# Kernel optimization log

Measured on AMD Instinct MI355X. Metric: run time of the kernel, lower is better.

The kernel has to match this reference:

```python
import jax, jax.numpy as jnp
import numpy as np

EPS = 1e-5

def masked_group_norm(x, mask, gamma, beta, num_groups):
    # x: [B,D,H,W,C] (zero at unoccupied), mask: [B,D,H,W,1] float
    B, D, H, W, C = x.shape
    G = num_groups
    Cg = C // G
    xg = x.reshape(B, -1, G, Cg)          # [B,V,G,Cg]
    m = mask.reshape(B, -1, 1, 1)         # [B,V,1,1]
    cnt = jnp.maximum(m.sum(axis=1, keepdims=True) * Cg, 1.0)  # elems per (B,G)
    mean = (xg * m).sum(axis=(1, 3), keepdims=True) / cnt
    var = (((xg - mean) ** 2) * m).sum(axis=(1, 3), keepdims=True) / cnt
    y = (xg - mean) * jax.lax.rsqrt(var + EPS)
    y = y.reshape(B, D, H, W, C)
    return (y * gamma + beta) * mask

def downsample2(x, mask):
    # mean-pool occupied children under coords//2; new site occupied if any child is
    B, D, H, W, C = x.shape
    xr = x.reshape(B, D // 2, 2, H // 2, 2, W // 2, 2, C)
    mr = mask.reshape(B, D // 2, 2, H // 2, 2, W // 2, 2, 1)
    cnt = mr.sum(axis=(2, 4, 6))
    y = xr.sum(axis=(2, 4, 6)) / jnp.maximum(cnt, 1.0)
    new_mask = (cnt > 0).astype(x.dtype)
    return y, new_mask

def subm_conv3d(x, w, b, mask):
    # submanifold conv: unoccupied inputs are zero; outputs only at occupied sites
    y = jax.lax.conv_general_dilated(
        x, w, window_strides=(1, 1, 1), padding='SAME',
        dimension_numbers=('NDHWC', 'DHWIO', 'NDHWC'))
    return (y + b) * mask

def setup_inputs() -> dict:
    key = jax.random.key(0)
    ks = jax.random.split(key, 12)
    B, D, C, Co = 4, 64, 64, 128
    x = jax.random.normal(ks[0], (B, D, D, D, C), dtype=jnp.float32)
    mask = jax.random.randint(ks[1], (B, D, D, D), 0, 2).astype(jnp.int32)
    s = 0.05
    return {
        'x': x, 'mask': mask,
        'gn1_w': jnp.ones((C,), jnp.float32), 'gn1_b': jnp.zeros((C,), jnp.float32),
        'w1': jax.random.normal(ks[2], (3, 3, 3, C, Co), jnp.float32) * s,
        'b1': jax.random.normal(ks[3], (Co,), jnp.float32) * s,
        'gn2_w': jnp.ones((Co,), jnp.float32), 'gn2_b': jnp.zeros((Co,), jnp.float32),
        'w2': jax.random.normal(ks[4], (3, 3, 3, Co, Co), jnp.float32) * s,
        'b2': jax.random.normal(ks[5], (Co,), jnp.float32) * s,
        'wskip': jax.random.normal(ks[6], (C, Co), jnp.float32) * s,
        'bskip': jax.random.normal(ks[7], (Co,), jnp.float32) * s,
    }

def reference(x, mask, gn1_w, gn1_b, w1, b1, gn2_w, gn2_b, w2, b2, wskip, bskip):
    NUM_GROUPS = 32
    m = mask.astype(x.dtype)[..., None]          # [B,D,H,W,1]
    x = x * m                                    # sparse tensor: zero off-mask
    # act_layers: SparseGroupNorm32 + SparseSiLU
    h = masked_group_norm(x, m, gn1_w, gn1_b, NUM_GROUPS)
    h = jax.nn.silu(h)                           # silu(0)=0, stays sparse
    # downsample both h and residual x
    h, dm = downsample2(h, m)
    xd, _ = downsample2(x, m)
    # out_layers: conv3 -> GN -> SiLU -> conv3
    h = subm_conv3d(h, w1, b1, dm)
    h = masked_group_norm(h, dm, gn2_w, gn2_b, NUM_GROUPS)
    h = jax.nn.silu(h)
    h = subm_conv3d(h, w2, b2, dm)
    # skip: 1x1 sparse conv (out_channels != channels)
    skip = (jnp.einsum('bdhwc,co->bdhwo', xd, wskip) + bskip) * dm
    return h + skip
```

## Files before the change

kernel.cpp:

```cpp
#include <hip/hip_runtime.h>
#include <cstdint>
#include <cstddef>

#define B_ 4
#define V1 262144
#define C1 64
#define V2 32768
#define C2 128
#define TOTV 131072
#define P_ 34
#define P2_ 1156
#define P3_ 39304
#define SBSTRIDE ((size_t)4 * P3_)

#define OFF_S1A 0
#define OFF_S2A 128
#define OFF_CNT1 256
#define OFF_S1B 260
#define OFF_S2B 388
#define OFF_CNT2 516

typedef __bf16 bf16x8 __attribute__((ext_vector_type(8)));
typedef float f32x4 __attribute__((ext_vector_type(4)));

__device__ __forceinline__ float bf2f(unsigned short u) {
    return __builtin_bit_cast(float, (unsigned)u << 16);
}
__device__ __forceinline__ unsigned short f2bf(float f) {
    unsigned u = __builtin_bit_cast(unsigned, f);
    u += 0x7fffu + ((u >> 16) & 1u);
    return (unsigned short)(u >> 16);
}
__device__ __forceinline__ float fast_silu(float x) {
    return x * __builtin_amdgcn_rcpf(1.f + __expf(-x));
}

__device__ __forceinline__ int a_ofs(int ks, int csh) {
    int s = ks & ((1 << csh) - 1), tap = ks >> csh;
    int dz = tap / 9, r = tap % 9, dy = r / 3, dx = r % 3;
    return s * (int)(SBSTRIDE * 64) + (dz * P2_ + dy * P_ + dx) * 64;
}

__global__ __launch_bounds__(256) void k0z_prep(const float* __restrict__ w1,
                                                const float* __restrict__ w2,
                                                const float* __restrict__ wskip,
                                                unsigned short* __restrict__ w1t,
                                                unsigned short* __restrict__ w2t,
                                                int* __restrict__ d1,
                                                int* __restrict__ d2,
                                                unsigned short* __restrict__ h1p,
                                                unsigned short* __restrict__ h2p)
{
    if (blockIdx.x >= 2624) {
        int i = (blockIdx.x - 2624) * 256 + threadIdx.x;
        if (i >= 24 * P3_) return;
        int sb = i / P3_, vox = i % P3_;
        int vz = vox / P2_, r = vox % P2_, vy = r / P_, vx = r % P_;
        bool border = (vz == 0) | (vz == 33) | (vy == 0) | (vy == 33) | (vx == 0) | (vx == 33);
        if (!border) return;
        unsigned short* base = (sb < 8) ? (h1p + (size_t)sb * P3_ * 32 + (size_t)vox * 32)
                                        : (h2p + (size_t)(sb - 8) * P3_ * 32 + (size_t)vox * 32);
        uint4 z = {0, 0, 0, 0};
        uint4* b4 = (uint4*)base;
        b4[0] = z; b4[1] = z; b4[2] = z; b4[3] = z;
        return;
    }
    int i = blockIdx.x * 256 + threadIdx.x;
    if (blockIdx.x == 0) {
        int t = threadIdx.x;
        if (t < 54)               d1[t] = (t + 1 < 54)  ? a_ofs(t + 1, 1) - a_ofs(t, 1) : 0;
        if (t >= 64 && t < 172) { int j = t - 64;
                                  d2[j] = (j + 1 < 108) ? a_ofs(j + 1, 2) - a_ofs(j, 2) : 0; }
    }
    if (i < 54 * 4096) {
        int slab = i >> 12, r = i & 4095;
        int q = r >> 10, n = (r >> 3) & 127, j = r & 7;
        int t = slab >> 1, s = slab & 1;
        int ci = s * 32 + q * 8 + j;
        w1t[i] = f2bf(w1[((size_t)t * 64 + ci) * 128 + n]);
    }
    int i2 = i - 54 * 4096;
    if (i2 >= 0 && i2 < 110 * 4096) {
        int slab = i2 >> 12, r = i2 & 4095;
        int q = r >> 10, n = (r >> 3) & 127, j = r & 7;
        float v;
        if (slab < 108) {
            int t = slab >> 2, s = slab & 3;
            int ci = s * 32 + q * 8 + j;
            v = w2[((size_t)t * 128 + ci) * 128 + n];
        } else {
            int ci = (slab - 108) * 32 + q * 8 + j;
            v = wskip[(size_t)ci * 128 + n];
        }
        w2t[i2] = f2bf(v);
    }
}

__global__ __launch_bounds__(256) void k1_stats1(const float* __restrict__ x,
                                                 const int* __restrict__ mask,
                                                 float* __restrict__ stats)
{
    __shared__ float ls1[32], ls2[32];
    __shared__ float lcnt;
    int tid = threadIdx.x;
    if (tid < 32) { ls1[tid] = 0.f; ls2[tid] = 0.f; }
    if (tid == 0) lcnt = 0.f;
    __syncthreads();

    int b  = blockIdx.x & 3;
    int bb = blockIdx.x >> 2;
    int c4 = tid & 15;
    int vl = tid >> 4;

    const float* xb = x + ((size_t)b * V1) * C1;
    const int*   mb = mask + (size_t)b * V1;

    float s1a = 0.f, s2a = 0.f, s1b = 0.f, s2b = 0.f, mc = 0.f;
    for (int ch = bb; ch < V1 / 16; ch += 1024) {
        int v = ch * 16 + vl;
        int m = mb[v];
        if (c4 == 0) mc += (float)m;
        if (m) {
            float4 xv = *(const float4*)(xb + (size_t)v * C1 + c4 * 4);
            s1a += xv.x + xv.y;  s2a += xv.x * xv.x + xv.y * xv.y;
            s1b += xv.z + xv.w;  s2b += xv.z * xv.z + xv.w * xv.w;
        }
    }
    atomicAdd(&ls1[2 * c4],     s1a); atomicAdd(&ls2[2 * c4],     s2a);
    atomicAdd(&ls1[2 * c4 + 1], s1b); atomicAdd(&ls2[2 * c4 + 1], s2b);
    if (c4 == 0) atomicAdd(&lcnt, mc);
    __syncthreads();
    if (tid < 32) {
        atomicAdd(&stats[OFF_S1A + b * 32 + tid], ls1[tid]);
        atomicAdd(&stats[OFF_S2A + b * 32 + tid], ls2[tid]);
    }
    if (tid == 0) atomicAdd(&stats[OFF_CNT1 + b], lcnt);
}

__global__ __launch_bounds__(256) void k2_down(const float* __restrict__ x,
                                               const int* __restrict__ mask,
                                               const float* __restrict__ gn1w,
                                               const float* __restrict__ gn1b,
                                               const float* __restrict__ stats,
                                               unsigned short* __restrict__ h1p,
                                               unsigned short* __restrict__ xdb,
                                               float* __restrict__ dm)
{
    int tid = threadIdx.x;
    int c  = tid & 63;
    int vl = tid >> 6;
    const size_t ovbase = (size_t)blockIdx.x * 32;
    const int b = (int)(ovbase >> 15);

    int g = c >> 1;
    float ce   = fmaxf(stats[OFF_CNT1 + b] * 2.f, 1.f);
    float mean = stats[OFF_S1A + b * 32 + g] / ce;
    float var  = stats[OFF_S2A + b * 32 + g] / ce - mean * mean;
    float rinv = rsqrtf(var + 1e-5f);
    float a  = rinv * gn1w[c];
    float bc = gn1b[c] - mean * a;

    const int*   mb = mask + ((size_t)b << 18);
    const float* xb = x + (((size_t)b << 18) << 6);

    #pragma unroll 2
    for (int it = 0; it < 8; ++it) {
        size_t ov = ovbase + it * 4 + vl;
        int v2 = (int)(ov & 32767);
        int z = v2 >> 10, y = (v2 >> 5) & 31, xk = v2 & 31;

        float hacc = 0.f, xacc = 0.f; int cnt = 0;
        #pragma unroll
        for (int dz = 0; dz < 2; ++dz)
        #pragma unroll
        for (int dy = 0; dy < 2; ++dy)
        #pragma unroll
        for (int dx = 0; dx < 2; ++dx) {
            int v1 = ((2 * z + dz) << 12) | ((2 * y + dy) << 6) | (2 * xk + dx);
            if (mb[v1]) {
                cnt++;
                float xv = xb[(size_t)v1 * 64 + c];
                xacc += xv;
                hacc += fast_silu(fmaf(xv, a, bc));
            }
        }
        float inv = __builtin_amdgcn_rcpf(fmaxf((float)cnt, 1.f));
        int pvox = (z + 1) * P2_ + (y + 1) * P_ + (xk + 1);
        size_t so = ((size_t)(c >> 5) * SBSTRIDE + (size_t)b * P3_ + pvox) * 32 + (c & 31);
        h1p[so] = f2bf(hacc * inv);
        xdb[ov * 64 + c] = f2bf(xacc * inv);
        if (c == 0) dm[ov] = (cnt > 0) ? 1.f : 0.f;
    }
}

template<int CIN, bool SKIP>
__global__ __launch_bounds__(256, 2) void conv3_mfma(
    const unsigned short* __restrict__ srcP,
    const unsigned short* __restrict__ sksrc,
    const unsigned short* __restrict__ wT,
    const int* __restrict__ tblA,
    const float* __restrict__ bias,
    const float* __restrict__ bias2,
    const float* __restrict__ dm,
    float* __restrict__ outf,
    unsigned short* __restrict__ outb)
{
    constexpr int CS   = CIN / 32;
    constexpr int NKM  = 27 * CS;
    constexpr int NPHM = NKM / 2;
    constexpr int NPH  = NPHM + (SKIP ? 1 : 0);

    __shared__ short smem[2][8192];

    const int tid  = threadIdx.x;
    const int lane = tid & 63;
    const int wv   = tid >> 6;
    const int orig = blockIdx.x;
    const int blk  = (orig & 7) * 64 + (orig >> 3);
    const int b    = blk >> 7;
    const int z    = (blk >> 2) & 31;
    const int yo   = blk & 3;
    const int y0   = yo * 8 + wv * 2;
    const int vb   = b * 32768;
    const int klo  = (lane >> 4) * 8;
    const int xl   = lane & 15;
    const int rlo  = (lane >> 4) * 4;

    f32x4 acc[4][8];
    #pragma unroll
    for (int f = 0; f < 4; ++f)
        #pragma unroll
        for (int nb = 0; nb < 8; ++nb)
            acc[f][nb] = (f32x4){0.f, 0.f, 0.f, 0.f};

    const char* pA = (const char*)srcP +
        (((size_t)b * P3_ + (size_t)(z * P2_ + y0 * P_ + xl)) * 32 + klo) * 2;

    auto loadSkip = [&](int ss, bf16x8* af) {
        const unsigned short* abase = sksrc + ss * 32;
        #pragma unroll
        for (int fy = 0; fy < 2; ++fy)
            #pragma unroll
            for (int fx = 0; fx < 2; ++fx)
                af[fy * 2 + fx] = *(const bf16x8*)(abase +
                    (size_t)(vb + z * 1024 + (y0 + fy) * 32 + fx * 16 + xl) * 64 + klo);
    };

    auto stageW = [&](int pr, int buf) {
        const char* g = (const char*)wT + (size_t)pr * 16384 + wv * 1024 + (lane << 4);
        char* l = (char*)&smem[0][0] + buf * 16384 + wv * 1024;
        #pragma unroll
        for (int j = 0; j < 4; ++j)
            __builtin_amdgcn_global_load_lds(
                (const __attribute__((address_space(1))) unsigned int*)(g + j * 4096),
                (__attribute__((address_space(3))) unsigned int*)(l + j * 4096),
                16, 0, 0);
    };

    auto loadAStep = [&](int ks, bf16x8* af) {
        af[0] = *(const bf16x8*)pA;
        af[1] = *(const bf16x8*)(pA + 1024);
        af[2] = *(const bf16x8*)(pA + 2176);
        af[3] = *(const bf16x8*)(pA + 3200);
        pA += tblA[ks];
    };

    bf16x8 afc[8];
    stageW(0, 0);
    loadAStep(0, &afc[0]);
    loadAStep(1, &afc[4]);
    asm volatile("s_waitcnt vmcnt(8)" ::: "memory");
    __builtin_amdgcn_s_barrier();

    int cur = 0;
    #pragma unroll 2
    for (int p = 0; p < NPH; ++p) {
        const bool more = (p + 1 < NPH);
        bf16x8 afn[8] = {{}, {}, {}, {}, {}, {}, {}, {}};
        if (more) {
            stageW(p + 1, cur ^ 1);
            if (2 * p + 2 < NKM) {
                loadAStep(2 * p + 2, &afn[0]);
                loadAStep(2 * p + 3, &afn[4]);
            } else if (SKIP) {
                loadSkip(0, &afn[0]);
                loadSkip(1, &afn[4]);
            }
        }
        __builtin_amdgcn_s_setprio(1);
        #pragma unroll
        for (int ss = 0; ss < 2; ++ss) {
            const short* bp = &smem[0][0] + cur * 8192 + ss * 4096 +
                              ((lane >> 4) * 128 + xl) * 8;
            #pragma unroll
            for (int nb = 0; nb < 8; ++nb) {
                bf16x8 bfr = *(const bf16x8*)(bp + nb * 128);
                acc[0][nb] = __builtin_amdgcn_mfma_f32_16x16x32_bf16(afc[ss * 4 + 0], bfr, acc[0][nb], 0, 0, 0);
                acc[1][nb] = __builtin_amdgcn_mfma_f32_16x16x32_bf16(afc[ss * 4 + 1], bfr, acc[1][nb], 0, 0, 0);
                acc[2][nb] = __builtin_amdgcn_mfma_f32_16x16x32_bf16(afc[ss * 4 + 2], bfr, acc[2][nb], 0, 0, 0);
                acc[3][nb] = __builtin_amdgcn_mfma_f32_16x16x32_bf16(afc[ss * 4 + 3], bfr, acc[3][nb], 0, 0, 0);
            }
        }
        __builtin_amdgcn_s_setprio(0);
        if (more) asm volatile("s_waitcnt vmcnt(8)" ::: "memory");
        else      asm volatile("s_waitcnt vmcnt(0)" ::: "memory");
        asm volatile("s_waitcnt lgkmcnt(0)" ::: "memory");
        __builtin_amdgcn_s_barrier();
        #pragma unroll
        for (int j = 0; j < 8; ++j) afc[j] = afn[j];
        cur ^= 1;
    }

    float bv[8];
    #pragma unroll
    for (int nb = 0; nb < 8; ++nb) {
        int co = nb * 16 + xl;
        if constexpr (SKIP) bv[nb] = bias[co] + bias2[co];
        else                bv[nb] = bias[co];
    }
    #pragma unroll
    for (int f = 0; f < 4; ++f) {
        const int fy = f >> 1, fx = f & 1;
        const int vox0 = vb + z * 1024 + (y0 + fy) * 32 + fx * 16 + rlo;
        float4 dm4 = *(const float4*)(dm + vox0);
        #pragma unroll
        for (int j = 0; j < 4; ++j) {
            const float dmx = (j == 0) ? dm4.x : (j == 1) ? dm4.y : (j == 2) ? dm4.z : dm4.w;
            const size_t obase = (size_t)(vox0 + j) * 128 + xl;
            #pragma unroll
            for (int nb = 0; nb < 8; ++nb) {
                float o = (acc[f][nb][j] + bv[nb]) * dmx;
                if constexpr (SKIP) outf[obase + nb * 16] = o;
                else                outb[obase + nb * 16] = f2bf(o);
            }
        }
    }
}

__global__ __launch_bounds__(256) void k4_stats2(const unsigned short* __restrict__ h2a,
                                                 const float* __restrict__ dm,
                                                 float* __restrict__ stats)
{
    __shared__ float ls1[32], ls2[32];
    __shared__ float lcnt;
    int tid = threadIdx.x;
    if (tid < 32) { ls1[tid] = 0.f; ls2[tid] = 0.f; }
    if (tid == 0) lcnt = 0.f;
    __syncthreads();

    int b  = blockIdx.x & 3;
    int bb = blockIdx.x >> 2;
    int g  = tid & 31;
    int vl = tid >> 5;

    const unsigned short* hb = h2a + ((size_t)b * V2) * C2;
    const float* dmb = dm + (size_t)b * V2;

    float s1 = 0.f, s2 = 0.f, mc = 0.f;
    for (int ch = bb; ch < V2 / 8; ch += 1024) {
        int v = ch * 8 + vl;
        float m = dmb[v];
        if (g == 0) mc += m;
        if (m != 0.f) {
            ushort4 hv = *(const ushort4*)(hb + (size_t)v * C2 + g * 4);
            float h0 = bf2f(hv.x), h1 = bf2f(hv.y), h2 = bf2f(hv.z), h3 = bf2f(hv.w);
            s1 += h0 + h1 + h2 + h3;
            s2 += h0 * h0 + h1 * h1 + h2 * h2 + h3 * h3;
        }
    }
    atomicAdd(&ls1[g], s1); atomicAdd(&ls2[g], s2);
    if (g == 0) atomicAdd(&lcnt, mc);
    __syncthreads();
    if (tid < 32) {
        atomicAdd(&stats[OFF_S1B + b * 32 + tid], ls1[tid]);
        atomicAdd(&stats[OFF_S2B + b * 32 + tid], ls2[tid]);
    }
    if (tid == 0) atomicAdd(&stats[OFF_CNT2 + b], lcnt);
}

__global__ __launch_bounds__(256) void k5_gn2(const unsigned short* __restrict__ h2a,
                                              unsigned short* __restrict__ h2p,
                                              const float* __restrict__ stats,
                                              const float* __restrict__ dm,
                                              const float* __restrict__ gn2w,
                                              const float* __restrict__ gn2b)
{
    int tid = threadIdx.x;
    int g = tid & 31;
    const int idx0 = blockIdx.x * 2048;
    const int b = (idx0 >> 5) >> 15;

    float ce   = fmaxf(stats[OFF_CNT2 + b] * 4.f, 1.f);
    float mean = stats[OFF_S1B + b * 32 + g] / ce;
    float var  = stats[OFF_S2B + b * 32 + g] / ce - mean * mean;
    float rinv = rsqrtf(var + 1e-5f);
    float4 gw = *(const float4*)(gn2w + g * 4);
    float4 gb = *(const float4*)(gn2b + g * 4);
    float ax = rinv * gw.x, bx = gb.x - mean * ax;
    float ay = rinv * gw.y, by = gb.y - mean * ay;
    float az = rinv * gw.z, bz = gb.z - mean * az;
    float aw = rinv * gw.w, bw = gb.w - mean * aw;

    #pragma unroll 2
    for (int it = 0; it < 8; ++it) {
        int idx = idx0 + it * 256 + tid;
        int v = idx >> 5;
        int v2 = v & 32767;
        float dmv = dm[v];
        ushort4 hv = *(const ushort4*)(h2a + (size_t)idx * 4);
        float t;
        ushort4 o;
        t = fmaf(bf2f(hv.x), ax, bx) * dmv; o.x = f2bf(fast_silu(t));
        t = fmaf(bf2f(hv.y), ay, by) * dmv; o.y = f2bf(fast_silu(t));
        t = fmaf(bf2f(hv.z), az, bz) * dmv; o.z = f2bf(fast_silu(t));
        t = fmaf(bf2f(hv.w), aw, bw) * dmv; o.w = f2bf(fast_silu(t));
        int zz = v2 >> 10, yy = (v2 >> 5) & 31, xx = v2 & 31;
        int pvox = (zz + 1) * P2_ + (yy + 1) * P_ + (xx + 1);
        size_t so = ((size_t)(g >> 3) * SBSTRIDE + (size_t)b * P3_ + pvox) * 32 + (g & 7) * 4;
        *(ushort4*)(h2p + so) = o;
    }
}

extern "C" void kernel_launch(void* const* d_in, const int* in_sizes, int n_in,
                              void* d_out, int out_size, void* d_ws, size_t ws_size,
                              hipStream_t stream)
{
    const float* x     = (const float*)d_in[0];
    const int*   mask  = (const int*)d_in[1];
    const float* gn1w  = (const float*)d_in[2];
    const float* gn1b  = (const float*)d_in[3];
    const float* w1    = (const float*)d_in[4];
    const float* b1    = (const float*)d_in[5];
    const float* gn2w  = (const float*)d_in[6];
    const float* gn2b  = (const float*)d_in[7];
    const float* w2    = (const float*)d_in[8];
    const float* b2    = (const float*)d_in[9];
    const float* wskip = (const float*)d_in[10];
    const float* bskip = (const float*)d_in[11];
    float* out = (float*)d_out;

    char* wsb = (char*)d_ws;
    float*          stats = (float*)wsb;
    float*          dm    = (float*)(wsb + 4096);
    unsigned short* h1p   = (unsigned short*)(wsb + 528384);
    unsigned short* xdb   = (unsigned short*)(wsb + 20652032);
    unsigned short* h2a   = (unsigned short*)(wsb + 37429248);
    unsigned short* h2p   = (unsigned short*)(wsb + 70983680);
    unsigned short* w1t   = (unsigned short*)(wsb + 111230976);
    unsigned short* w2t   = (unsigned short*)(wsb + 111673344);
    int*            d1    = (int*)(wsb + 112574464);
    int*            d2    = (int*)(wsb + 112574720);

    hipMemsetAsync(stats, 0, 520 * sizeof(float), stream);

    hipLaunchKernelGGL(k0z_prep, dim3(2624 + 3685), dim3(256), 0, stream,
                       w1, w2, wskip, w1t, w2t, d1, d2, h1p, h2p);
    hipLaunchKernelGGL(k1_stats1, dim3(4096), dim3(256), 0, stream, x, mask, stats);
    hipLaunchKernelGGL(k2_down, dim3(4096), dim3(256), 0, stream,
                       x, mask, gn1w, gn1b, stats, h1p, xdb, dm);
    hipLaunchKernelGGL((conv3_mfma<64, false>), dim3(512), dim3(256), 0, stream,
                       h1p, (const unsigned short*)nullptr, w1t, d1, b1, (const float*)nullptr,
                       dm, (float*)nullptr, h2a);
    hipLaunchKernelGGL(k4_stats2, dim3(4096), dim3(256), 0, stream, h2a, dm, stats);
    hipLaunchKernelGGL(k5_gn2, dim3(2048), dim3(256), 0, stream, h2a, h2p, stats, dm, gn2w, gn2b);
    hipLaunchKernelGGL((conv3_mfma<128, true>), dim3(512), dim3(256), 0, stream,
                       h2p, xdb, w2t, d2, b2, bskip, dm, out, (unsigned short*)nullptr);
}
```

Before: 418.3 us.

## Fuse GN2 statistics into conv1 epilogue and write padded layout directly

The first conv's epilogue now writes its bf16 output straight into the padded, channel-sliced layout used by conv2, and accumulates per-group sum and sum-of-squares via wave shuffles and LDS atomics. This removes the separate stats2 kernel and its read of the intermediate. The occupancy count moves into the downsample kernel. GN2 then normalizes in place on the padded buffer. The cost is extra epilogue work and atomics in conv1, plus scattered stores into the padded layout.

New measurement: 374.4 us. -10.5%, faster.

```diff
diff --git a/kernel.cpp b/kernel.cpp
--- a/kernel.cpp
+++ b/kernel.cpp
@@ -141,12 +141,15 @@
                                                const int* __restrict__ mask,
                                                const float* __restrict__ gn1w,
                                                const float* __restrict__ gn1b,
-                                               const float* __restrict__ stats,
+                                               float* __restrict__ stats,
                                                unsigned short* __restrict__ h1p,
                                                unsigned short* __restrict__ xdb,
                                                float* __restrict__ dm)
 {
+    __shared__ float bcnt;
     int tid = threadIdx.x;
+    if (tid == 0) bcnt = 0.f;
+    __syncthreads();
     int c  = tid & 63;
     int vl = tid >> 6;
     const size_t ovbase = (size_t)blockIdx.x * 32;
@@ -163,6 +166,7 @@
     const int*   mb = mask + ((size_t)b << 18);
     const float* xb = x + (((size_t)b << 18) << 6);
 
+    float mycnt = 0.f;
     #pragma unroll 2
     for (int it = 0; it < 8; ++it) {
         size_t ov = ovbase + it * 4 + vl;
@@ -189,8 +193,15 @@
         size_t so = ((size_t)(c >> 5) * SBSTRIDE + (size_t)b * P3_ + pvox) * 32 + (c & 31);
         h1p[so] = f2bf(hacc * inv);
         xdb[ov * 64 + c] = f2bf(xacc * inv);
-        if (c == 0) dm[ov] = (cnt > 0) ? 1.f : 0.f;
-    }
+        if (c == 0) {
+            float d = (cnt > 0) ? 1.f : 0.f;
+            dm[ov] = d;
+            mycnt += d;
+        }
+    }
+    if (c == 0) atomicAdd(&bcnt, mycnt);
+    __syncthreads();
+    if (tid == 0) atomicAdd(&stats[OFF_CNT2 + b], bcnt);
 }
 
 template<int CIN, bool SKIP>
@@ -203,7 +214,8 @@
     const float* __restrict__ bias2,
     const float* __restrict__ dm,
     float* __restrict__ outf,
-    unsigned short* __restrict__ outb)
+    unsigned short* __restrict__ outb,
+    float* __restrict__ statsOut)
 {
     constexpr int CS   = CIN / 32;
     constexpr int NKM  = 27 * CS;
@@ -318,68 +330,75 @@
         if constexpr (SKIP) bv[nb] = bias[co] + bias2[co];
         else                bv[nb] = bias[co];
     }
-    #pragma unroll
-    for (int f = 0; f < 4; ++f) {
-        const int fy = f >> 1, fx = f & 1;
-        const int vox0 = vb + z * 1024 + (y0 + fy) * 32 + fx * 16 + rlo;
-        float4 dm4 = *(const float4*)(dm + vox0);
-        #pragma unroll
-        for (int j = 0; j < 4; ++j) {
-            const float dmx = (j == 0) ? dm4.x : (j == 1) ? dm4.y : (j == 2) ? dm4.z : dm4.w;
-            const size_t obase = (size_t)(vox0 + j) * 128 + xl;
+    if constexpr (SKIP) {
+        #pragma unroll
+        for (int f = 0; f < 4; ++f) {
+            const int fy = f >> 1, fx = f & 1;
+            const int vox0 = vb + z * 1024 + (y0 + fy) * 32 + fx * 16 + rlo;
+            float4 dm4 = *(const float4*)(dm + vox0);
             #pragma unroll
-            for (int nb = 0; nb < 8; ++nb) {
-                float o = (acc[f][nb][j] + bv[nb]) * dmx;
-                if constexpr (SKIP) outf[obase + nb * 16] = o;
-                else                outb[obase + nb * 16] = f2bf(o);
-            }
-        }
-    }
-}
-
-__global__ __launch_bounds__(256) void k4_stats2(const unsigned short* __restrict__ h2a,
-                                                 const float* __restrict__ dm,
-                                                 float* __restrict__ stats)
-{
-    __shared__ float ls1[32], ls2[32];
-    __shared__ float lcnt;
-    int tid = threadIdx.x;
-    if (tid < 32) { ls1[tid] = 0.f; ls2[tid] = 0.f; }
-    if (tid == 0) lcnt = 0.f;
-    __syncthreads();
-
-    int b  = blockIdx.x & 3;
-    int bb = blockIdx.x >> 2;
-    int g  = tid & 31;
-    int vl = tid >> 5;
-
-    const unsigned short* hb = h2a + ((size_t)b * V2) * C2;
-    const float* dmb = dm + (size_t)b * V2;
-
-    float s1 = 0.f, s2 = 0.f, mc = 0.f;
-    for (int ch = bb; ch < V2 / 8; ch += 1024) {
-        int v = ch * 8 + vl;
-        float m = dmb[v];
-        if (g == 0) mc += m;
-        if (m != 0.f) {
-            ushort4 hv = *(const ushort4*)(hb + (size_t)v * C2 + g * 4);
-            float h0 = bf2f(hv.x), h1 = bf2f(hv.y), h2 = bf2f(hv.z), h3 = bf2f(hv.w);
-            s1 += h0 + h1 + h2 + h3;
-            s2 += h0 * h0 + h1 * h1 + h2 * h2 + h3 * h3;
-        }
-    }
-    atomicAdd(&ls1[g], s1); atomicAdd(&ls2[g], s2);
-    if (g == 0) atomicAdd(&lcnt, mc);
-    __syncthreads();
-    if (tid < 32) {
-        atomicAdd(&stats[OFF_S1B + b * 32 + tid], ls1[tid]);
-        atomicAdd(&stats[OFF_S2B + b * 32 + tid], ls2[tid]);
-    }
-    if (tid == 0) atomicAdd(&stats[OFF_CNT2 + b], lcnt);
-}
-
-__global__ __launch_bounds__(256) void k5_gn2(const unsigned short* __restrict__ h2a,
-                                              unsigned short* __restrict__ h2p,
+            for (int j = 0; j < 4; ++j) {
+                const float dmx = (j == 0) ? dm4.x : (j == 1) ? dm4.y : (j == 2) ? dm4.z : dm4.w;
+                const size_t obase = (size_t)(vox0 + j) * 128 + xl;
+                #pragma unroll
+                for (int nb = 0; nb < 8; ++nb) {
+                    float o = (acc[f][nb][j] + bv[nb]) * dmx;
+                    outf[obase + nb * 16] = o;
+                }
+            }
+        }
+    } else {
+        float ps1[8], ps2[8];
+        #pragma unroll
+        for (int nb = 0; nb < 8; ++nb) { ps1[nb] = 0.f; ps2[nb] = 0.f; }
+        #pragma unroll
+        for (int f = 0; f < 4; ++f) {
+            const int fy = f >> 1, fx = f & 1;
+            const int yrow = y0 + fy;
+            const int xc0  = fx * 16 + rlo;
+            const int vox0 = vb + z * 1024 + yrow * 32 + xc0;
+            float4 dm4 = *(const float4*)(dm + vox0);
+            #pragma unroll
+            for (int j = 0; j < 4; ++j) {
+                const float dmx = (j == 0) ? dm4.x : (j == 1) ? dm4.y : (j == 2) ? dm4.z : dm4.w;
+                const int pvox = (z + 1) * P2_ + (yrow + 1) * P_ + (xc0 + j + 1);
+                const size_t sbase = (size_t)b * P3_ + pvox;
+                #pragma unroll
+                for (int nb = 0; nb < 8; ++nb) {
+                    float o = (acc[f][nb][j] + bv[nb]) * dmx;
+                    int co = nb * 16 + xl;
+                    size_t so = ((size_t)(co >> 5) * SBSTRIDE + sbase) * 32 + (co & 31);
+                    outb[so] = f2bf(o);
+                    ps1[nb] += o; ps2[nb] += o * o;
+                }
+            }
+        }
+        float* lsum = (float*)&smem[0][0];
+        __syncthreads();
+        if (tid < 64) lsum[tid] = 0.f;
+        __syncthreads();
+        #pragma unroll
+        for (int nb = 0; nb < 8; ++nb) {
+            float s1 = ps1[nb], s2 = ps2[nb];
+            s1 += __shfl_xor(s1, 1);  s2 += __shfl_xor(s2, 1);
+            s1 += __shfl_xor(s1, 2);  s2 += __shfl_xor(s2, 2);
+            s1 += __shfl_xor(s1, 16); s2 += __shfl_xor(s2, 16);
+            s1 += __shfl_xor(s1, 32); s2 += __shfl_xor(s2, 32);
+            if ((lane & 0x33) == 0) {
+                int g = nb * 4 + (xl >> 2);
+                atomicAdd(&lsum[g], s1);
+                atomicAdd(&lsum[32 + g], s2);
+            }
+        }
+        __syncthreads();
+        if (tid < 32) {
+            atomicAdd(&statsOut[OFF_S1B + b * 32 + tid], lsum[tid]);
+            atomicAdd(&statsOut[OFF_S2B + b * 32 + tid], lsum[32 + tid]);
+        }
+    }
+}
+
+__global__ __launch_bounds__(256) void k5_gn2(unsigned short* __restrict__ h2p,
                                               const float* __restrict__ stats,
                                               const float* __restrict__ dm,
                                               const float* __restrict__ gn2w,
@@ -407,16 +426,16 @@
         int v = idx >> 5;
         int v2 = v & 32767;
         float dmv = dm[v];
-        ushort4 hv = *(const ushort4*)(h2a + (size_t)idx * 4);
+        int zz = v2 >> 10, yy = (v2 >> 5) & 31, xx = v2 & 31;
+        int pvox = (zz + 1) * P2_ + (yy + 1) * P_ + (xx + 1);
+        size_t so = ((size_t)(g >> 3) * SBSTRIDE + (size_t)b * P3_ + pvox) * 32 + (g & 7) * 4;
+        ushort4 hv = *(const ushort4*)(h2p + so);
         float t;
         ushort4 o;
         t = fmaf(bf2f(hv.x), ax, bx) * dmv; o.x = f2bf(fast_silu(t));
         t = fmaf(bf2f(hv.y), ay, by) * dmv; o.y = f2bf(fast_silu(t));
         t = fmaf(bf2f(hv.z), az, bz) * dmv; o.z = f2bf(fast_silu(t));
         t = fmaf(bf2f(hv.w), aw, bw) * dmv; o.w = f2bf(fast_silu(t));
-        int zz = v2 >> 10, yy = (v2 >> 5) & 31, xx = v2 & 31;
-        int pvox = (zz + 1) * P2_ + (yy + 1) * P_ + (xx + 1);
-        size_t so = ((size_t)(g >> 3) * SBSTRIDE + (size_t)b * P3_ + pvox) * 32 + (g & 7) * 4;
         *(ushort4*)(h2p + so) = o;
     }
 }
@@ -444,7 +463,6 @@
     float*          dm    = (float*)(wsb + 4096);
     unsigned short* h1p   = (unsigned short*)(wsb + 528384);
     unsigned short* xdb   = (unsigned short*)(wsb + 20652032);
-    unsigned short* h2a   = (unsigned short*)(wsb + 37429248);
     unsigned short* h2p   = (unsigned short*)(wsb + 70983680);
     unsigned short* w1t   = (unsigned short*)(wsb + 111230976);
     unsigned short* w2t   = (unsigned short*)(wsb + 111673344);
@@ -460,9 +478,9 @@
                        x, mask, gn1w, gn1b, stats, h1p, xdb, dm);
     hipLaunchKernelGGL((conv3_mfma<64, false>), dim3(512), dim3(256), 0, stream,
                        h1p, (const unsigned short*)nullptr, w1t, d1, b1, (const float*)nullptr,
-                       dm, (float*)nullptr, h2a);
-    hipLaunchKernelGGL(k4_stats2, dim3(4096), dim3(256), 0, stream, h2a, dm, stats);
-    hipLaunchKernelGGL(k5_gn2, dim3(2048), dim3(256), 0, stream, h2a, h2p, stats, dm, gn2w, gn2b);
+                       dm, (float*)nullptr, h2p, stats);
+    hipLaunchKernelGGL(k5_gn2, dim3(2048), dim3(256), 0, stream, h2p, stats, dm, gn2w, gn2b);
     hipLaunchKernelGGL((conv3_mfma<128, true>), dim3(512), dim3(256), 0, stream,
-                       h2p, xdb, w2t, d2, b2, bskip, dm, out, (unsigned short*)nullptr);
-}
+                       h2p, xdb, w2t, d2, b2, bskip, dm, out, (unsigned short*)nullptr,
+                       (float*)nullptr);
+}
```
